# Kernel tuning notes

Measured on AMD Instinct MI355X. Metric: run time of the kernel, lower is better.

The kernel has to match this reference:

```python
import jax, jax.numpy as jnp
import numpy as np

B, T, D = 4, 2048, 768
H = 12
HD = D // H
WINDOW = 128

def setup_inputs() -> dict:
    key = jax.random.key(0)
    k1, k2, k3 = jax.random.split(key, 3)
    x = jax.random.normal(k1, (B, T, D), dtype=jnp.float32)
    Wqkv = jax.random.normal(k2, (D, 3 * D), dtype=jnp.float32) * 0.02
    Wout = jax.random.normal(k3, (D, D), dtype=jnp.float32) * 0.02
    return {"x": x, "Wqkv": Wqkv, "Wout": Wout}

def reference(x, Wqkv, Wout):
    Bx, Tx, Dx = x.shape
    qkv = x @ Wqkv                      # [B,T,3D]
    q, k, v = jnp.split(qkv, 3, axis=-1)
    def heads(t):
        return t.reshape(Bx, Tx, H, HD).transpose(0, 2, 1, 3)  # [B,H,T,hd]
    q, k, v = heads(q), heads(k), heads(v)
    scale = 1.0 / jnp.sqrt(jnp.float32(HD))
    scores = jnp.einsum('bhqd,bhkd->bhqk', q, k) * scale       # [B,H,T,T]
    pos = jnp.arange(Tx)
    dist = pos[None, :] - pos[:, None]                          # j - i
    blocked = (dist > 0) | (dist < -WINDOW)                     # causal band
    scores = jnp.where(blocked[None, None], -jnp.inf, scores)
    attn = jax.nn.softmax(scores, axis=-1)
    out = jnp.einsum('bhqk,bhkd->bhqd', attn, v)                # [B,H,T,hd]
    out = out.transpose(0, 2, 1, 3).reshape(Bx, Tx, Dx)
    return out @ Wout
```

## Files before the change

kernel.cpp:

```cpp
#include <hip/hip_runtime.h>
#include <hip/hip_bf16.h>
#include <stdint.h>

typedef unsigned short u16;
typedef __attribute__((ext_vector_type(8))) short short8;
typedef __attribute__((ext_vector_type(8))) __bf16 bf16x8;
typedef __attribute__((ext_vector_type(4))) float f32x4;

constexpr int Bc  = 4;
constexpr int Tc  = 2048;
constexpr int Dc  = 768;
constexpr int Hc  = 12;
constexpr int WINc = 128;

static __device__ __forceinline__ u16 f2bf(float f) {
  union { float f; uint32_t u; } v; v.f = f;
  uint32_t u = v.u;
  return (u16)((u + 0x7fffu + ((u >> 16) & 1u)) >> 16);
}

static __device__ __forceinline__ f32x4 mfma16x16x32(bf16x8 a, bf16x8 b, f32x4 c) {
  return __builtin_amdgcn_mfma_f32_16x16x32_bf16(a, b, c, 0, 0, 0);
}

#define GLOAD_LDS16(gsrc, ldst)                                                \
  __builtin_amdgcn_global_load_lds(                                            \
      (const __attribute__((address_space(1))) void*)(gsrc),                   \
      (__attribute__((address_space(3))) void*)(ldst), 16, 0, 0)

__global__ __launch_bounds__(256) void prep(const float* __restrict__ x,
                                            u16* __restrict__ xb,
                                            const float* __restrict__ Wqkv,
                                            u16* __restrict__ wqkvT,
                                            const float* __restrict__ Wout,
                                            u16* __restrict__ woutT) {
  __shared__ float tile[64][65];
  const int t = threadIdx.x;
  const int b = blockIdx.x;
  if (b < 6144) {
    const int i = b * 256 + t;
    const float4 f = ((const float4*)x)[i];
    union { u16 h[4]; uint2 u; } pk;
    pk.h[0] = f2bf(f.x); pk.h[1] = f2bf(f.y); pk.h[2] = f2bf(f.z); pk.h[3] = f2bf(f.w);
    ((uint2*)xb)[i] = pk.u;
    return;
  }
  const float* W; u16* WT; int C, bx, by;
  if (b < 6576) { W = Wqkv; WT = wqkvT; C = 2304; const int bb = b - 6144; bx = bb % 36; by = bb / 36; }
  else          { W = Wout; WT = woutT; C = 768;  const int bb = b - 6576; bx = bb % 12; by = bb / 12; }
  const int R = 768;
  const int c0 = bx * 64, r0 = by * 64;
#pragma unroll
  for (int i = 0; i < 16; ++i) {
    const int e = i * 256 + t;
    const int r = e >> 6, c = e & 63;
    tile[r][c] = W[(size_t)(r0 + r) * C + c0 + c];
  }
  __syncthreads();
#pragma unroll
  for (int i = 0; i < 16; ++i) {
    const int e = i * 256 + t;
    const int r = e >> 6, c = e & 63;
    WT[(size_t)(c0 + r) * R + r0 + c] = f2bf(tile[c][r]);
  }
}

template <int EPI>
__global__ __launch_bounds__(256) void gemm_bt(const u16* __restrict__ A,
                                               const u16* __restrict__ Bt,
                                               u16* __restrict__ q_ws,
                                               u16* __restrict__ k_ws,
                                               u16* __restrict__ v_ws,
                                               float* __restrict__ fout) {
  __shared__ u16 As[2][128][64];
  __shared__ u16 Bs[2][128][64];
  const int t  = threadIdx.x;
  const int w  = t >> 6, l = t & 63;
  const int lr = l & 15, lh = l >> 4;
  const int wm = w >> 1, wn = w & 1;
  const int m0 = blockIdx.y * 128, n0 = blockIdx.x * 128;

  f32x4 acc[4][4];
#pragma unroll
  for (int mi = 0; mi < 4; ++mi)
#pragma unroll
    for (int ni = 0; ni < 4; ++ni) acc[mi][ni] = f32x4{0.f, 0.f, 0.f, 0.f};

  const int srow = w * 8 + (l >> 3);
  const int scol = ((l & 7) ^ (l >> 3)) * 8;
  const u16* aP = A  + (size_t)(m0 + srow) * 768 + scol;
  const u16* bP = Bt + (size_t)(n0 + srow) * 768 + scol;

#define STAGE(kt, b)                                                           \
  {                                                                            \
    const int ko_ = (kt) * 64;                                                 \
    char* asB_ = (char*)As + (b) * 16384 + w * 1024;                           \
    char* bsB_ = (char*)Bs + (b) * 16384 + w * 1024;                           \
    _Pragma("unroll")                                                          \
    for (int j = 0; j < 4; ++j) {                                              \
      GLOAD_LDS16(aP + ko_ + j * (32 * 768), asB_ + j * 4096);                 \
      GLOAD_LDS16(bP + ko_ + j * (32 * 768), bsB_ + j * 4096);                 \
    }                                                                          \
  }

#define COMPUTE(b)                                                             \
  {                                                                            \
    _Pragma("unroll")                                                          \
    for (int kk = 0; kk < 2; ++kk) {                                           \
      const int cb = (kk * 64 + lh * 16) ^ ((lr & 7) << 4);                    \
      bf16x8 af[4], bfr[4];                                                    \
      _Pragma("unroll")                                                        \
      for (int mi = 0; mi < 4; ++mi)                                           \
        af[mi] = *(const bf16x8*)((const char*)As + (b) * 16384 +              \
                                  (wm * 64 + mi * 16 + lr) * 128 + cb);        \
      _Pragma("unroll")                                                        \
      for (int ni = 0; ni < 4; ++ni)                                           \
        bfr[ni] = *(const bf16x8*)((const char*)Bs + (b) * 16384 +             \
                                   (wn * 64 + ni * 16 + lr) * 128 + cb);       \
      _Pragma("unroll")                                                        \
      for (int mi = 0; mi < 4; ++mi)                                           \
        _Pragma("unroll")                                                      \
        for (int ni = 0; ni < 4; ++ni)                                         \
          acc[mi][ni] = mfma16x16x32(af[mi], bfr[ni], acc[mi][ni]);            \
    }                                                                          \
  }

  STAGE(0, 0);
  for (int kt = 0; kt < 11; ++kt) {
    const int b = kt & 1;
    STAGE(kt + 1, b ^ 1);
    asm volatile("s_waitcnt vmcnt(8)" ::: "memory");
    __builtin_amdgcn_sched_barrier(0);
    __builtin_amdgcn_s_barrier();
    COMPUTE(b);
    __builtin_amdgcn_s_barrier();
  }
  asm volatile("s_waitcnt vmcnt(0)" ::: "memory");
  __builtin_amdgcn_sched_barrier(0);
  __builtin_amdgcn_s_barrier();
  COMPUTE(1);

#undef STAGE
#undef COMPUTE

  if (EPI == 0) {
#pragma unroll
    for (int mi = 0; mi < 4; ++mi)
#pragma unroll
      for (int ni = 0; ni < 4; ++ni) {
        const int col   = n0 + wn * 64 + ni * 16 + lr;
        const int which = col / 768;
        const int rem   = col - which * 768;
        const int h     = rem >> 6, d = rem & 63;
        u16* dst = (which == 0) ? q_ws : ((which == 1) ? k_ws : v_ws);
        const float scl = (which == 0) ? 0.125f : 1.0f;
#pragma unroll
        for (int r = 0; r < 4; ++r) {
          const int m  = m0 + wm * 64 + mi * 16 + lh * 4 + r;
          const int bb = m >> 11, tt = m & 2047;
          dst[(((size_t)(bb * Hc + h) * Tc + tt) << 6) + d] = f2bf(acc[mi][ni][r] * scl);
        }
      }
  } else {
#pragma unroll
    for (int mi = 0; mi < 4; ++mi)
#pragma unroll
      for (int ni = 0; ni < 4; ++ni) {
        const int col = n0 + wn * 64 + ni * 16 + lr;
#pragma unroll
        for (int r = 0; r < 4; ++r) {
          const int m = m0 + wm * 64 + mi * 16 + lh * 4 + r;
          fout[(size_t)m * 768 + col] = acc[mi][ni][r];
        }
      }
  }
}

__global__ __launch_bounds__(256) void swa_attn(const u16* __restrict__ Q,
                                                const u16* __restrict__ Kk,
                                                const u16* __restrict__ V,
                                                u16* __restrict__ Out) {
  __shared__ u16 Ks[3][64][72];
  __shared__ u16 Vt[3][64][72];
  __shared__ u16 Ps[4][16][72];

  const int t  = threadIdx.x;
  const int w  = t >> 6, l = t & 63;
  const int lr = l & 15, lh = l >> 4;
  const int bh = blockIdx.y;
  const int q0 = blockIdx.x * 64;
  const size_t hb = (size_t)bh * Tc * 64;

  const int kb_lo = (q0 >= WINc) ? q0 - WINc : 0;
  const int nt    = ((q0 - kb_lo) >> 6) + 1;

  const u16* qrow = Q + hb + (size_t)(q0 + w * 16 + lr) * 64;
  const bf16x8 qa0 = *(const bf16x8*)(qrow + lh * 8);
  const bf16x8 qa1 = *(const bf16x8*)(qrow + 32 + lh * 8);

  const int row = t >> 2, c = (t & 3) * 16;
  short8 kreg[3][2], vreg[3][2];
#pragma unroll
  for (int ti = 0; ti < 3; ++ti) {
    if (ti < nt) {
      const int kb = kb_lo + ti * 64;
      const short8* ksrc = (const short8*)(Kk + hb + (size_t)(kb + row) * 64 + c);
      const short8* vsrc = (const short8*)(V  + hb + (size_t)(kb + row) * 64 + c);
      kreg[ti][0] = ksrc[0]; kreg[ti][1] = ksrc[1];
      vreg[ti][0] = vsrc[0]; vreg[ti][1] = vsrc[1];
    }
  }
#pragma unroll
  for (int ti = 0; ti < 3; ++ti) {
    if (ti < nt) {
      *(short8*)&Ks[ti][row][c]     = kreg[ti][0];
      *(short8*)&Ks[ti][row][c + 8] = kreg[ti][1];
#pragma unroll
      for (int j = 0; j < 8; ++j) {
        Vt[ti][c + j][row]     = (u16)vreg[ti][0][j];
        Vt[ti][c + 8 + j][row] = (u16)vreg[ti][1][j];
      }
    }
  }
  __syncthreads();

  const short8 ones_i = {(short)0x3F80, (short)0x3F80, (short)0x3F80, (short)0x3F80,
                         (short)0x3F80, (short)0x3F80, (short)0x3F80, (short)0x3F80};
  const bf16x8 onesv = *(const bf16x8*)&ones_i;

  float m_r[4];
  f32x4 lacc = f32x4{0.f, 0.f, 0.f, 0.f};
  f32x4 Oa[4];
#pragma unroll
  for (int r = 0; r < 4; ++r) m_r[r] = -1e30f;
#pragma unroll
  for (int n = 0; n < 4; ++n) Oa[n] = f32x4{0.f, 0.f, 0.f, 0.f};

#pragma unroll
  for (int ti = 0; ti < 3; ++ti) {
    if (ti >= nt) break;
    const int kb = kb_lo + ti * 64;

    f32x4 s[4];
#pragma unroll
    for (int sub = 0; sub < 4; ++sub) {
      const bf16x8 kb0 = *(const bf16x8*)&Ks[ti][sub * 16 + lr][lh * 8];
      const bf16x8 kb1 = *(const bf16x8*)&Ks[ti][sub * 16 + lr][32 + lh * 8];
      f32x4 z = f32x4{0.f, 0.f, 0.f, 0.f};
      z = mfma16x16x32(qa0, kb0, z);
      z = mfma16x16x32(qa1, kb1, z);
      s[sub] = z;
    }

    const int qbase = q0 + w * 16 + lh * 4;
#pragma unroll
    for (int sub = 0; sub < 4; ++sub) {
      const int kj = kb + sub * 16 + lr;
#pragma unroll
      for (int r = 0; r < 4; ++r) {
        const int qi = qbase + r;
        const bool ok = (kj <= qi) && (kj + WINc >= qi);
        s[sub][r] = ok ? s[sub][r] : -1e30f;
      }
    }

    float mt[4];
#pragma unroll
    for (int r = 0; r < 4; ++r)
      mt[r] = fmaxf(fmaxf(s[0][r], s[1][r]), fmaxf(s[2][r], s[3][r]));
#pragma unroll
    for (int msk = 1; msk < 16; msk <<= 1)
#pragma unroll
      for (int r = 0; r < 4; ++r)
        mt[r] = fmaxf(mt[r], __shfl_xor(mt[r], msk, 64));

    float al[4];
#pragma unroll
    for (int r = 0; r < 4; ++r) {
      const float mn = fmaxf(m_r[r], mt[r]);
      al[r] = __expf(m_r[r] - mn);
      m_r[r] = mn;
    }

#pragma unroll
    for (int sub = 0; sub < 4; ++sub)
#pragma unroll
      for (int r = 0; r < 4; ++r)
        s[sub][r] = __expf(s[sub][r] - m_r[r]);

#pragma unroll
    for (int n = 0; n < 4; ++n)
#pragma unroll
      for (int r = 0; r < 4; ++r) Oa[n][r] *= al[r];
#pragma unroll
    for (int r = 0; r < 4; ++r) lacc[r] *= al[r];

#pragma unroll
    for (int sub = 0; sub < 4; ++sub)
#pragma unroll
      for (int r = 0; r < 4; ++r)
        Ps[w][lh * 4 + r][sub * 16 + lr] = f2bf(s[sub][r]);

#pragma unroll
    for (int ks = 0; ks < 2; ++ks) {
      const bf16x8 pa = *(const bf16x8*)&Ps[w][lr][ks * 32 + lh * 8];
      lacc = mfma16x16x32(pa, onesv, lacc);
#pragma unroll
      for (int n = 0; n < 4; ++n) {
        const bf16x8 vb = *(const bf16x8*)&Vt[ti][n * 16 + lr][ks * 32 + lh * 8];
        Oa[n] = mfma16x16x32(pa, vb, Oa[n]);
      }
    }
  }

  const int bb = bh / Hc, h = bh - bb * Hc;
#pragma unroll
  for (int r = 0; r < 4; ++r) {
    const float inv = 1.f / lacc[r];
    const int ti = q0 + w * 16 + lh * 4 + r;
#pragma unroll
    for (int n = 0; n < 4; ++n)
      Out[((size_t)(bb * Tc + ti)) * 768 + h * 64 + n * 16 + lr] =
          f2bf(Oa[n][r] * inv);
  }
}

extern "C" void kernel_launch(void* const* d_in, const int* in_sizes, int n_in,
                              void* d_out, int out_size, void* d_ws, size_t ws_size,
                              hipStream_t stream) {
  (void)in_sizes; (void)n_in; (void)out_size; (void)ws_size;
  const float* x    = (const float*)d_in[0];
  const float* Wqkv = (const float*)d_in[1];
  const float* Wout = (const float*)d_in[2];
  float* out = (float*)d_out;

  u16* ws    = (u16*)d_ws;
  u16* xb    = ws;
  u16* wqkvT = xb + 6291456;
  u16* woutT = wqkvT + 1769472;
  u16* qws   = woutT + 589824;
  u16* kws   = qws + 6291456;
  u16* vws   = kws + 6291456;
  u16* aws   = xb;

  prep<<<6720, 256, 0, stream>>>(x, xb, Wqkv, wqkvT, Wout, woutT);
  gemm_bt<0><<<dim3(18, 64), 256, 0, stream>>>(xb, wqkvT, qws, kws, vws, nullptr);
  swa_attn<<<dim3(32, 48), 256, 0, stream>>>(qws, kws, vws, aws);
  gemm_bt<1><<<dim3(6, 64), 256, 0, stream>>>(aws, woutT, nullptr, nullptr, nullptr, out);
}
```

Measured before the change: 103.6 us.

## Widen attention query tile to 128 rows and skip out-of-window KV tiles per subtile

Each attention block now handles 128 queries (32 per wave, as two 16-row subtiles) and loads 4 KV tiles instead of 3. K/V loads per query are amortised better, and each 16-row subtile only visits the KV tiles that intersect its causal window, cutting masked MFMA work. LDS padding also changes from 72 to 68 columns. In exchange the grid has half as many blocks (768), which lowers parallelism, and LDS use grows, which may reduce occupancy.

```diff
diff --git a/kernel.cpp b/kernel.cpp
--- a/kernel.cpp
+++ b/kernel.cpp
@@ -180,45 +180,54 @@
                                                 const u16* __restrict__ Kk,
                                                 const u16* __restrict__ V,
                                                 u16* __restrict__ Out) {
-  __shared__ u16 Ks[3][64][72];
-  __shared__ u16 Vt[3][64][72];
-  __shared__ u16 Ps[4][16][72];
+  __shared__ u16 Ks[4][64][68];
+  __shared__ u16 Vt[4][64][68];
+  __shared__ u16 Ps[4][16][68];
 
   const int t  = threadIdx.x;
   const int w  = t >> 6, l = t & 63;
   const int lr = l & 15, lh = l >> 4;
   const int bh = blockIdx.y;
-  const int q0 = blockIdx.x * 64;
+  const int q0 = blockIdx.x * 128;
   const size_t hb = (size_t)bh * Tc * 64;
 
-  const int kb_lo = (q0 >= WINc) ? q0 - WINc : 0;
-  const int nt    = ((q0 - kb_lo) >> 6) + 1;
-
-  const u16* qrow = Q + hb + (size_t)(q0 + w * 16 + lr) * 64;
-  const bf16x8 qa0 = *(const bf16x8*)(qrow + lh * 8);
-  const bf16x8 qa1 = *(const bf16x8*)(qrow + 32 + lh * 8);
+  const int tile_base = (q0 >= 128) ? q0 - 128 : 0;
+  const int nt = ((q0 + 64 - tile_base) >> 6) + 1;
+
+  const u16* qp = Q + hb + (size_t)(q0 + w * 32 + lr) * 64;
+  bf16x8 qa[2][2];
+#pragma unroll
+  for (int qs = 0; qs < 2; ++qs) {
+    qa[qs][0] = *(const bf16x8*)(qp + (size_t)qs * 16 * 64 + lh * 8);
+    qa[qs][1] = *(const bf16x8*)(qp + (size_t)qs * 16 * 64 + 32 + lh * 8);
+  }
 
   const int row = t >> 2, c = (t & 3) * 16;
-  short8 kreg[3][2], vreg[3][2];
-#pragma unroll
-  for (int ti = 0; ti < 3; ++ti) {
-    if (ti < nt) {
-      const int kb = kb_lo + ti * 64;
-      const short8* ksrc = (const short8*)(Kk + hb + (size_t)(kb + row) * 64 + c);
-      const short8* vsrc = (const short8*)(V  + hb + (size_t)(kb + row) * 64 + c);
-      kreg[ti][0] = ksrc[0]; kreg[ti][1] = ksrc[1];
-      vreg[ti][0] = vsrc[0]; vreg[ti][1] = vsrc[1];
+#pragma unroll
+  for (int half = 0; half < 2; ++half) {
+    short8 kreg[2][2], vreg[2][2];
+#pragma unroll
+    for (int i = 0; i < 2; ++i) {
+      const int ti = half * 2 + i;
+      if (ti < nt) {
+        const int kb = tile_base + ti * 64;
+        const short8* ksrc = (const short8*)(Kk + hb + (size_t)(kb + row) * 64 + c);
+        const short8* vsrc = (const short8*)(V  + hb + (size_t)(kb + row) * 64 + c);
+        kreg[i][0] = ksrc[0]; kreg[i][1] = ksrc[1];
+        vreg[i][0] = vsrc[0]; vreg[i][1] = vsrc[1];
+      }
     }
-  }
-#pragma unroll
-  for (int ti = 0; ti < 3; ++ti) {
-    if (ti < nt) {
-      *(short8*)&Ks[ti][row][c]     = kreg[ti][0];
-      *(short8*)&Ks[ti][row][c + 8] = kreg[ti][1];
-#pragma unroll
-      for (int j = 0; j < 8; ++j) {
-        Vt[ti][c + j][row]     = (u16)vreg[ti][0][j];
-        Vt[ti][c + 8 + j][row] = (u16)vreg[ti][1][j];
+#pragma unroll
+    for (int i = 0; i < 2; ++i) {
+      const int ti = half * 2 + i;
+      if (ti < nt) {
+        *(short8*)&Ks[ti][row][c]     = kreg[i][0];
+        *(short8*)&Ks[ti][row][c + 8] = kreg[i][1];
+#pragma unroll
+        for (int j = 0; j < 8; ++j) {
+          Vt[ti][c + j][row]     = (u16)vreg[i][0][j];
+          Vt[ti][c + 8 + j][row] = (u16)vreg[i][1][j];
+        }
       }
     }
   }
@@ -227,101 +236,106 @@
   const short8 ones_i = {(short)0x3F80, (short)0x3F80, (short)0x3F80, (short)0x3F80,
                          (short)0x3F80, (short)0x3F80, (short)0x3F80, (short)0x3F80};
   const bf16x8 onesv = *(const bf16x8*)&ones_i;
-
-  float m_r[4];
-  f32x4 lacc = f32x4{0.f, 0.f, 0.f, 0.f};
-  f32x4 Oa[4];
-#pragma unroll
-  for (int r = 0; r < 4; ++r) m_r[r] = -1e30f;
-#pragma unroll
-  for (int n = 0; n < 4; ++n) Oa[n] = f32x4{0.f, 0.f, 0.f, 0.f};
-
-#pragma unroll
-  for (int ti = 0; ti < 3; ++ti) {
-    if (ti >= nt) break;
-    const int kb = kb_lo + ti * 64;
-
-    f32x4 s[4];
-#pragma unroll
-    for (int sub = 0; sub < 4; ++sub) {
-      const bf16x8 kb0 = *(const bf16x8*)&Ks[ti][sub * 16 + lr][lh * 8];
-      const bf16x8 kb1 = *(const bf16x8*)&Ks[ti][sub * 16 + lr][32 + lh * 8];
-      f32x4 z = f32x4{0.f, 0.f, 0.f, 0.f};
-      z = mfma16x16x32(qa0, kb0, z);
-      z = mfma16x16x32(qa1, kb1, z);
-      s[sub] = z;
+  const int bb = bh / Hc, h = bh - bb * Hc;
+
+  for (int qs = 0; qs < 2; ++qs) {
+    const int qglob = q0 + w * 32 + qs * 16;
+    const int lo    = (qglob >= 128) ? (qglob - 128) : 0;
+    const int ti_lo = ((lo & ~63) - tile_base) >> 6;
+    const int ti_hi = ((qglob & ~63) - tile_base) >> 6;
+
+    float m_r[4];
+    f32x4 lacc = f32x4{0.f, 0.f, 0.f, 0.f};
+    f32x4 Oa[4];
+#pragma unroll
+    for (int r = 0; r < 4; ++r) m_r[r] = -1e30f;
+#pragma unroll
+    for (int n = 0; n < 4; ++n) Oa[n] = f32x4{0.f, 0.f, 0.f, 0.f};
+
+    for (int ti = ti_lo; ti <= ti_hi; ++ti) {
+      const int kb = tile_base + ti * 64;
+
+      f32x4 s[4];
+#pragma unroll
+      for (int sub = 0; sub < 4; ++sub) {
+        const bf16x8 kb0 = *(const bf16x8*)&Ks[ti][sub * 16 + lr][lh * 8];
+        const bf16x8 kb1 = *(const bf16x8*)&Ks[ti][sub * 16 + lr][32 + lh * 8];
+        f32x4 z = f32x4{0.f, 0.f, 0.f, 0.f};
+        z = mfma16x16x32(qa[qs][0], kb0, z);
+        z = mfma16x16x32(qa[qs][1], kb1, z);
+        s[sub] = z;
+      }
+
+      const int qbase = qglob + lh * 4;
+#pragma unroll
+      for (int sub = 0; sub < 4; ++sub) {
+        const int kj = kb + sub * 16 + lr;
+#pragma unroll
+        for (int r = 0; r < 4; ++r) {
+          const int qi = qbase + r;
+          const bool ok = (kj <= qi) && (kj + WINc >= qi);
+          s[sub][r] = ok ? s[sub][r] : -1e30f;
+        }
+      }
+
+      float mt[4];
+#pragma unroll
+      for (int r = 0; r < 4; ++r)
+        mt[r] = fmaxf(fmaxf(s[0][r], s[1][r]), fmaxf(s[2][r], s[3][r]));
+#pragma unroll
+      for (int msk = 1; msk < 16; msk <<= 1)
+#pragma unroll
+        for (int r = 0; r < 4; ++r)
+          mt[r] = fmaxf(mt[r], __shfl_xor(mt[r], msk, 64));
+
+      float al[4];
+#pragma unroll
+      for (int r = 0; r < 4; ++r) {
+        const float mn = fmaxf(m_r[r], mt[r]);
+        al[r] = __expf(m_r[r] - mn);
+        m_r[r] = mn;
+      }
+
+#pragma unroll
+      for (int sub = 0; sub < 4; ++sub)
+#pragma unroll
+        for (int r = 0; r < 4; ++r)
+          s[sub][r] = __expf(s[sub][r] - m_r[r]);
+
+#pragma unroll
+      for (int n = 0; n < 4; ++n)
+#pragma unroll
+        for (int r = 0; r < 4; ++r) Oa[n][r] *= al[r];
+#pragma unroll
+      for (int r = 0; r < 4; ++r) lacc[r] *= al[r];
+
+#pragma unroll
+      for (int sub = 0; sub < 4; ++sub)
+#pragma unroll
+        for (int r = 0; r < 4; ++r)
+          Ps[w][lh * 4 + r][sub * 16 + lr] = f2bf(s[sub][r]);
+
+#pragma unroll
+      for (int ks = 0; ks < 2; ++ks) {
+        const bf16x8 pa = *(const bf16x8*)&Ps[w][lr][ks * 32 + lh * 8];
+        lacc = mfma16x16x32(pa, onesv, lacc);
+#pragma unroll
+        for (int n = 0; n < 4; ++n) {
+          const bf16x8 vb = *(const bf16x8*)&Vt[ti][n * 16 + lr][ks * 32 + lh * 8];
+          Oa[n] = mfma16x16x32(pa, vb, Oa[n]);
+        }
+      }
     }
 
-    const int qbase = q0 + w * 16 + lh * 4;
-#pragma unroll
-    for (int sub = 0; sub < 4; ++sub) {
-      const int kj = kb + sub * 16 + lr;
-#pragma unroll
-      for (int r = 0; r < 4; ++r) {
-        const int qi = qbase + r;
-        const bool ok = (kj <= qi) && (kj + WINc >= qi);
-        s[sub][r] = ok ? s[sub][r] : -1e30f;
-      }
+#pragma unroll
+    for (int r = 0; r < 4; ++r) {
+      const float inv = 1.f / lacc[r];
+      const int ti_o = qglob + lh * 4 + r;
+#pragma unroll
+      for (int n = 0; n < 4; ++n)
+        Out[((size_t)(bb * Tc + ti_o)) * 768 + h * 64 + n * 16 + lr] =
+            f2bf(Oa[n][r] * inv);
     }
-
-    float mt[4];
-#pragma unroll
-    for (int r = 0; r < 4; ++r)
-      mt[r] = fmaxf(fmaxf(s[0][r], s[1][r]), fmaxf(s[2][r], s[3][r]));
-#pragma unroll
-    for (int msk = 1; msk < 16; msk <<= 1)
-#pragma unroll
-      for (int r = 0; r < 4; ++r)
-        mt[r] = fmaxf(mt[r], __shfl_xor(mt[r], msk, 64));
-
-    float al[4];
-#pragma unroll
-    for (int r = 0; r < 4; ++r) {
-      const float mn = fmaxf(m_r[r], mt[r]);
-      al[r] = __expf(m_r[r] - mn);
-      m_r[r] = mn;
-    }
-
-#pragma unroll
-    for (int sub = 0; sub < 4; ++sub)
-#pragma unroll
-      for (int r = 0; r < 4; ++r)
-        s[sub][r] = __expf(s[sub][r] - m_r[r]);
-
-#pragma unroll
-    for (int n = 0; n < 4; ++n)
-#pragma unroll
-      for (int r = 0; r < 4; ++r) Oa[n][r] *= al[r];
-#pragma unroll
-    for (int r = 0; r < 4; ++r) lacc[r] *= al[r];
-
-#pragma unroll
-    for (int sub = 0; sub < 4; ++sub)
-#pragma unroll
-      for (int r = 0; r < 4; ++r)
-        Ps[w][lh * 4 + r][sub * 16 + lr] = f2bf(s[sub][r]);
-
-#pragma unroll
-    for (int ks = 0; ks < 2; ++ks) {
-      const bf16x8 pa = *(const bf16x8*)&Ps[w][lr][ks * 32 + lh * 8];
-      lacc = mfma16x16x32(pa, onesv, lacc);
-#pragma unroll
-      for (int n = 0; n < 4; ++n) {
-        const bf16x8 vb = *(const bf16x8*)&Vt[ti][n * 16 + lr][ks * 32 + lh * 8];
-        Oa[n] = mfma16x16x32(pa, vb, Oa[n]);
-      }
-    }
-  }
-
-  const int bb = bh / Hc, h = bh - bb * Hc;
-#pragma unroll
-  for (int r = 0; r < 4; ++r) {
-    const float inv = 1.f / lacc[r];
-    const int ti = q0 + w * 16 + lh * 4 + r;
-#pragma unroll
-    for (int n = 0; n < 4; ++n)
-      Out[((size_t)(bb * Tc + ti)) * 768 + h * 64 + n * 16 + lr] =
-          f2bf(Oa[n][r] * inv);
   }
 }
 
@@ -345,6 +359,6 @@
 
   prep<<<6720, 256, 0, stream>>>(x, xb, Wqkv, wqkvT, Wout, woutT);
   gemm_bt<0><<<dim3(18, 64), 256, 0, stream>>>(xb, wqkvT, qws, kws, vws, nullptr);
-  swa_attn<<<dim3(32, 48), 256, 0, stream>>>(qws, kws, vws, aws);
+  swa_attn<<<dim3(16, 48), 256, 0, stream>>>(qws, kws, vws, aws);
   gemm_bt<1><<<dim3(6, 64), 256, 0, stream>>>(aws, woutT, nullptr, nullptr, nullptr, out);
 }
```

Result: slower. 118.2 us (+14.1%).

## Use single-pass softmax over full window and swizzle transposed V in LDS

Applied to the files above, without the earlier changes.

The attention kernel now computes scores for all key tiles up front and takes one row max, so the per-tile rescaling of the output and row-sum accumulators goes away. The transposed V stores into shared memory are XOR-swizzled to cut bank conflicts on the scalar transpose writes. The P staging buffer is double-buffered across tiles, which may remove a read-after-write hazard. In exchange, all score tiles stay live in registers at once, which raises register pressure and may lower occupancy.

```diff
diff --git a/kernel.cpp b/kernel.cpp
--- a/kernel.cpp
+++ b/kernel.cpp
@@ -182,7 +182,7 @@
                                                 u16* __restrict__ Out) {
   __shared__ u16 Ks[3][64][72];
   __shared__ u16 Vt[3][64][72];
-  __shared__ u16 Ps[4][16][72];
+  __shared__ u16 Ps[2][4][16][72];
 
   const int t  = threadIdx.x;
   const int w  = t >> 6, l = t & 63;
@@ -215,10 +215,11 @@
     if (ti < nt) {
       *(short8*)&Ks[ti][row][c]     = kreg[ti][0];
       *(short8*)&Ks[ti][row][c + 8] = kreg[ti][1];
+      const int rsw = row ^ c;
 #pragma unroll
       for (int j = 0; j < 8; ++j) {
-        Vt[ti][c + j][row]     = (u16)vreg[ti][0][j];
-        Vt[ti][c + 8 + j][row] = (u16)vreg[ti][1][j];
+        Vt[ti][c + j][rsw]     = (u16)vreg[ti][0][j];
+        Vt[ti][c + 8 + j][rsw] = (u16)vreg[ti][1][j];
       }
     }
   }
@@ -228,87 +229,91 @@
                          (short)0x3F80, (short)0x3F80, (short)0x3F80, (short)0x3F80};
   const bf16x8 onesv = *(const bf16x8*)&ones_i;
 
+  f32x4 s[3][4];
+#pragma unroll
+  for (int ti = 0; ti < 3; ++ti) {
+    if (ti < nt) {
+#pragma unroll
+      for (int sub = 0; sub < 4; ++sub) {
+        const bf16x8 kb0 = *(const bf16x8*)&Ks[ti][sub * 16 + lr][lh * 8];
+        const bf16x8 kb1 = *(const bf16x8*)&Ks[ti][sub * 16 + lr][32 + lh * 8];
+        f32x4 z = f32x4{0.f, 0.f, 0.f, 0.f};
+        z = mfma16x16x32(qa0, kb0, z);
+        z = mfma16x16x32(qa1, kb1, z);
+        s[ti][sub] = z;
+      }
+    }
+  }
+
+  const int qbase = q0 + w * 16 + lh * 4;
+#pragma unroll
+  for (int ti = 0; ti < 3; ++ti) {
+    if (ti < nt) {
+      const int kb = kb_lo + ti * 64;
+#pragma unroll
+      for (int sub = 0; sub < 4; ++sub) {
+        const int kj = kb + sub * 16 + lr;
+#pragma unroll
+        for (int r = 0; r < 4; ++r) {
+          const int qi = qbase + r;
+          const bool ok = (kj <= qi) && (kj + WINc >= qi);
+          s[ti][sub][r] = ok ? s[ti][sub][r] : -1e30f;
+        }
+      }
+    }
+  }
+
   float m_r[4];
+#pragma unroll
+  for (int r = 0; r < 4; ++r) m_r[r] = -1e30f;
+#pragma unroll
+  for (int ti = 0; ti < 3; ++ti)
+    if (ti < nt)
+#pragma unroll
+      for (int sub = 0; sub < 4; ++sub)
+#pragma unroll
+        for (int r = 0; r < 4; ++r)
+          m_r[r] = fmaxf(m_r[r], s[ti][sub][r]);
+#pragma unroll
+  for (int msk = 1; msk < 16; msk <<= 1)
+#pragma unroll
+    for (int r = 0; r < 4; ++r)
+      m_r[r] = fmaxf(m_r[r], __shfl_xor(m_r[r], msk, 64));
+
+#pragma unroll
+  for (int ti = 0; ti < 3; ++ti)
+    if (ti < nt)
+#pragma unroll
+      for (int sub = 0; sub < 4; ++sub)
+#pragma unroll
+        for (int r = 0; r < 4; ++r)
+          s[ti][sub][r] = __expf(s[ti][sub][r] - m_r[r]);
+
   f32x4 lacc = f32x4{0.f, 0.f, 0.f, 0.f};
   f32x4 Oa[4];
 #pragma unroll
-  for (int r = 0; r < 4; ++r) m_r[r] = -1e30f;
-#pragma unroll
   for (int n = 0; n < 4; ++n) Oa[n] = f32x4{0.f, 0.f, 0.f, 0.f};
 
 #pragma unroll
   for (int ti = 0; ti < 3; ++ti) {
-    if (ti >= nt) break;
-    const int kb = kb_lo + ti * 64;
-
-    f32x4 s[4];
-#pragma unroll
-    for (int sub = 0; sub < 4; ++sub) {
-      const bf16x8 kb0 = *(const bf16x8*)&Ks[ti][sub * 16 + lr][lh * 8];
-      const bf16x8 kb1 = *(const bf16x8*)&Ks[ti][sub * 16 + lr][32 + lh * 8];
-      f32x4 z = f32x4{0.f, 0.f, 0.f, 0.f};
-      z = mfma16x16x32(qa0, kb0, z);
-      z = mfma16x16x32(qa1, kb1, z);
-      s[sub] = z;
-    }
-
-    const int qbase = q0 + w * 16 + lh * 4;
-#pragma unroll
-    for (int sub = 0; sub < 4; ++sub) {
-      const int kj = kb + sub * 16 + lr;
-#pragma unroll
-      for (int r = 0; r < 4; ++r) {
-        const int qi = qbase + r;
-        const bool ok = (kj <= qi) && (kj + WINc >= qi);
-        s[sub][r] = ok ? s[sub][r] : -1e30f;
-      }
-    }
-
-    float mt[4];
-#pragma unroll
-    for (int r = 0; r < 4; ++r)
-      mt[r] = fmaxf(fmaxf(s[0][r], s[1][r]), fmaxf(s[2][r], s[3][r]));
-#pragma unroll
-    for (int msk = 1; msk < 16; msk <<= 1)
-#pragma unroll
-      for (int r = 0; r < 4; ++r)
-        mt[r] = fmaxf(mt[r], __shfl_xor(mt[r], msk, 64));
-
-    float al[4];
-#pragma unroll
-    for (int r = 0; r < 4; ++r) {
-      const float mn = fmaxf(m_r[r], mt[r]);
-      al[r] = __expf(m_r[r] - mn);
-      m_r[r] = mn;
-    }
-
-#pragma unroll
-    for (int sub = 0; sub < 4; ++sub)
-#pragma unroll
-      for (int r = 0; r < 4; ++r)
-        s[sub][r] = __expf(s[sub][r] - m_r[r]);
-
-#pragma unroll
-    for (int n = 0; n < 4; ++n)
-#pragma unroll
-      for (int r = 0; r < 4; ++r) Oa[n][r] *= al[r];
-#pragma unroll
-    for (int r = 0; r < 4; ++r) lacc[r] *= al[r];
-
-#pragma unroll
-    for (int sub = 0; sub < 4; ++sub)
-#pragma unroll
-      for (int r = 0; r < 4; ++r)
-        Ps[w][lh * 4 + r][sub * 16 + lr] = f2bf(s[sub][r]);
-
-#pragma unroll
-    for (int ks = 0; ks < 2; ++ks) {
-      const bf16x8 pa = *(const bf16x8*)&Ps[w][lr][ks * 32 + lh * 8];
-      lacc = mfma16x16x32(pa, onesv, lacc);
-#pragma unroll
-      for (int n = 0; n < 4; ++n) {
-        const bf16x8 vb = *(const bf16x8*)&Vt[ti][n * 16 + lr][ks * 32 + lh * 8];
-        Oa[n] = mfma16x16x32(pa, vb, Oa[n]);
+    if (ti < nt) {
+      const int pb = ti & 1;
+#pragma unroll
+      for (int sub = 0; sub < 4; ++sub)
+#pragma unroll
+        for (int r = 0; r < 4; ++r)
+          Ps[pb][w][lh * 4 + r][sub * 16 + lr] = f2bf(s[ti][sub][r]);
+
+#pragma unroll
+      for (int ks = 0; ks < 2; ++ks) {
+        const bf16x8 pa = *(const bf16x8*)&Ps[pb][w][lr][ks * 32 + lh * 8];
+        lacc = mfma16x16x32(pa, onesv, lacc);
+#pragma unroll
+        for (int n = 0; n < 4; ++n) {
+          const bf16x8 vb =
+              *(const bf16x8*)&Vt[ti][n * 16 + lr][(ks * 32 + lh * 8) ^ (n * 16)];
+          Oa[n] = mfma16x16x32(pa, vb, Oa[n]);
+        }
       }
     }
   }
@@ -317,10 +322,10 @@
 #pragma unroll
   for (int r = 0; r < 4; ++r) {
     const float inv = 1.f / lacc[r];
-    const int ti = q0 + w * 16 + lh * 4 + r;
+    const int ti_o = q0 + w * 16 + lh * 4 + r;
 #pragma unroll
     for (int n = 0; n < 4; ++n)
-      Out[((size_t)(bb * Tc + ti)) * 768 + h * 64 + n * 16 + lr] =
+      Out[((size_t)(bb * Tc + ti_o)) * 768 + h * 64 + n * 16 + lr] =
           f2bf(Oa[n][r] * inv);
   }
 }
```

New measurement: 103.1 us. Within noise of the previous version (-0.5%).
